# Kernel optimization log

Measured on AMD Instinct MI355X. Metric: run time of the kernel, lower is better.

## Reference

```python
import jax, jax.numpy as jnp
import numpy as np

N = 100000
E = 1600000
IN_F = 128
OUT_F = 64
ALPHA = 0.2  # leaky relu slope
EPS = 1e-16


def setup_inputs() -> dict:
    key = jax.random.key(0)
    k1, k2, k3, k4 = jax.random.split(key, 4)
    x = jax.random.normal(k1, (N, IN_F), dtype=jnp.float32)
    edge_index = jax.random.randint(k2, (2, E), 0, N, dtype=jnp.int64)
    # xavier_uniform with gain=1.414
    gain = 1.414
    limW = gain * np.sqrt(6.0 / (IN_F + OUT_F))
    W = jax.random.uniform(k3, (IN_F, OUT_F), minval=-limW, maxval=limW, dtype=jnp.float32)
    lima = gain * np.sqrt(6.0 / (2 * OUT_F + 1))
    a = jax.random.uniform(k4, (2 * OUT_F, 1), minval=-lima, maxval=lima, dtype=jnp.float32)
    return {"x": x, "edge_index": edge_index, "W": W, "a": a}


def reference(x, edge_index, W, a):
    src = edge_index[0]
    tgt = edge_index[1]
    Wh = x @ W  # (N, out)
    # e = leakyrelu([Wh[src] || Wh[tgt]] @ a) ; split a to avoid materializing concat
    a_src = a[:OUT_F, 0]
    a_tgt = a[OUT_F:, 0]
    score_src = Wh @ a_src  # (N,)
    score_tgt = Wh @ a_tgt  # (N,)
    e = jax.nn.leaky_relu(score_src[src] + score_tgt[tgt], ALPHA)  # (E,)
    # segment softmax over edges grouped by target node
    e_max = jax.ops.segment_max(e, tgt, num_segments=N)  # -inf for empty segments, never gathered
    e_exp = jnp.exp(e - e_max[tgt])
    e_sum = jax.ops.segment_sum(e_exp, tgt, num_segments=N)
    alpha = e_exp / (e_sum[tgt] + EPS)  # (E,)
    # dropout is identity in eval mode
    v_weighted = Wh[src] * alpha[:, None]  # (E, out)
    h_prime = jax.ops.segment_sum(v_weighted, tgt, num_segments=N)  # (N, out)
    return jax.nn.elu(h_prime)  # concat=True branch
```

## Files before the change

kernel.cpp:

```cpp
#include <hip/hip_runtime.h>

#define N_NODES 100000
#define N_EDGES 1600000
#define IN_FEAT 128
#define OUT_FEAT 64
#define LRELU_SLOPE 0.2f
#define EPS_DENOM 1e-16f

#define SB_SHIFT 8
#define SB_NODES 256
#define NSB 391
#define N_SUB 8
#define SUBA_CAP 704
#define STAGE_CAP 4608
#define CH 4096
#define SCAT_BLOCKS ((N_EDGES + CH - 1) / CH)
#define GEMM_BLOCKS ((N_NODES + 63) / 64)

typedef __attribute__((ext_vector_type(8))) short bf16x8;
typedef __attribute__((ext_vector_type(4))) float f32x4;

__device__ __forceinline__ unsigned int enc_f(float x) {
    unsigned int u = __float_as_uint(x);
    return (u & 0x80000000u) ? ~u : (u | 0x80000000u);
}
__device__ __forceinline__ float dec_f(unsigned int u) {
    u = (u & 0x80000000u) ? (u ^ 0x80000000u) : ~u;
    return __uint_as_float(u);
}
#define ENC_NEG_INF 0x007FFFFFu

__device__ __forceinline__ unsigned short f2bf(float f) {
    unsigned int u = __float_as_uint(f);
    u = (u + 0x7FFFu + ((u >> 16) & 1u)) >> 16;
    return (unsigned short)u;
}

__global__ __launch_bounds__(256) void init_prep_kernel(
    const float* __restrict__ W, int* __restrict__ cursorA,
    unsigned short* __restrict__ WTb)
{
    const int i = blockIdx.x * 256 + threadIdx.x;
    if (i < NSB * N_SUB) cursorA[i] = i * SUBA_CAP;
    if (i < OUT_FEAT * IN_FEAT) {
        const int n = i >> 7, k = i & 127;
        WTb[i] = f2bf(W[k * OUT_FEAT + n]);
    }
}

struct GemmS {
    unsigned short xs[64][136];
    float ssp[4][64];
    float stp[4][64];
};
struct ScatS {
    int staged[CH];
    int hcnt[NSB];
    int gbase[NSB];
    int lcnt[NSB];
    int lbase[NSB];
    int pfx[256];
};

__global__ __launch_bounds__(256) void gemm_scatter_kernel(
    const float* __restrict__ x, const unsigned short* __restrict__ WTb,
    const float* __restrict__ a, const int* __restrict__ ei,
    int* __restrict__ cursorA, int* __restrict__ bucketsA,
    unsigned short* __restrict__ WhB,
    float* __restrict__ s_src, float* __restrict__ s_tgt)
{
    __shared__ __align__(16) char smem[sizeof(ScatS) > sizeof(GemmS) ? sizeof(ScatS)
                                                                     : sizeof(GemmS)];
    const int tid = threadIdx.x;

    if (blockIdx.x < SCAT_BLOCKS) {
        ScatS& S = *(ScatS*)smem;
        const int base = blockIdx.x * CH;
        const int sub = blockIdx.x & (N_SUB - 1);
        for (int j = tid; j < NSB; j += 256) S.hcnt[j] = 0;
        __syncthreads();
        int tloc[CH / 256], sloc[CH / 256];
        #pragma unroll
        for (int k = 0; k < CH / 256; ++k) {
            const int i = base + k * 256 + tid;
            tloc[k] = (i < N_EDGES) ? ei[N_EDGES + i] : -1;
            sloc[k] = (i < N_EDGES) ? ei[i] : 0;
            if (tloc[k] >= 0) atomicAdd(&S.hcnt[tloc[k] >> SB_SHIFT], 1);
        }
        __syncthreads();
        int carry = 0;
        for (int c0 = 0; c0 < NSB; c0 += 256) {
            const int idx = c0 + tid;
            const int v = (idx < NSB) ? S.hcnt[idx] : 0;
            S.pfx[tid] = v;
            __syncthreads();
            for (int off = 1; off < 256; off <<= 1) {
                const int add = (tid >= off) ? S.pfx[tid - off] : 0;
                __syncthreads();
                S.pfx[tid] += add;
                __syncthreads();
            }
            if (idx < NSB) S.lbase[idx] = carry + S.pfx[tid] - v;
            carry += S.pfx[255];
            __syncthreads();
        }
        for (int j = tid; j < NSB; j += 256) {
            S.lcnt[j] = 0;
            const int c = S.hcnt[j];
            S.gbase[j] = c ? atomicAdd(&cursorA[j * N_SUB + sub], c) : 0;
        }
        __syncthreads();
        #pragma unroll
        for (int k = 0; k < CH / 256; ++k) {
            if (tloc[k] >= 0) {
                const int sb = tloc[k] >> SB_SHIFT;
                const int r = atomicAdd(&S.lcnt[sb], 1);
                S.staged[S.lbase[sb] + r] = sloc[k] | ((tloc[k] & (SB_NODES - 1)) << 17);
            }
        }
        __syncthreads();
        const int grp = tid >> 4, gl = tid & 15;
        for (int sb = grp; sb < NSB; sb += 16) {
            const int c = S.hcnt[sb];
            const int lb = S.lbase[sb];
            const int gb = S.gbase[sb];
            for (int k = gl; k < c; k += 16) bucketsA[gb + k] = S.staged[lb + k];
        }
        return;
    }

    GemmS& G = *(GemmS*)smem;
    const int wid = tid >> 6, lane = tid & 63;
    const int r0 = (blockIdx.x - SCAT_BLOCKS) * 64;

    #pragma unroll
    for (int it = 0; it < 8; ++it) {
        const int idx4 = it * 256 + tid;
        const int row = idx4 >> 5;
        const int col = (idx4 & 31) * 4;
        float4 v = make_float4(0.f, 0.f, 0.f, 0.f);
        if (r0 + row < N_NODES) v = *(const float4*)(x + (size_t)(r0 + row) * IN_FEAT + col);
        const unsigned int p0 = (unsigned int)f2bf(v.x) | ((unsigned int)f2bf(v.y) << 16);
        const unsigned int p1 = (unsigned int)f2bf(v.z) | ((unsigned int)f2bf(v.w) << 16);
        *(uint2*)&G.xs[row][col] = make_uint2(p0, p1);
    }
    __syncthreads();

    const int cgrp = lane >> 4;
    const int cl = lane & 15;
    const int col = wid * 16 + cl;
    f32x4 acc0 = {0.f,0.f,0.f,0.f}, acc1 = acc0, acc2 = acc0, acc3 = acc0;
    #pragma unroll
    for (int kb = 0; kb < IN_FEAT; kb += 32) {
        const bf16x8 bfrag = *(const bf16x8*)(WTb + col * IN_FEAT + kb + cgrp * 8);
        const bf16x8 a0 = *(const bf16x8*)&G.xs[ 0 + cl][kb + cgrp * 8];
        const bf16x8 a1 = *(const bf16x8*)&G.xs[16 + cl][kb + cgrp * 8];
        const bf16x8 a2 = *(const bf16x8*)&G.xs[32 + cl][kb + cgrp * 8];
        const bf16x8 a3 = *(const bf16x8*)&G.xs[48 + cl][kb + cgrp * 8];
        acc0 = __builtin_amdgcn_mfma_f32_16x16x32_bf16(a0, bfrag, acc0, 0, 0, 0);
        acc1 = __builtin_amdgcn_mfma_f32_16x16x32_bf16(a1, bfrag, acc1, 0, 0, 0);
        acc2 = __builtin_amdgcn_mfma_f32_16x16x32_bf16(a2, bfrag, acc2, 0, 0, 0);
        acc3 = __builtin_amdgcn_mfma_f32_16x16x32_bf16(a3, bfrag, acc3, 0, 0, 0);
    }

    const float a_s = a[col], a_t = a[OUT_FEAT + col];
    #pragma unroll
    for (int mt = 0; mt < 4; ++mt) {
        const f32x4 av = (mt == 0) ? acc0 : (mt == 1) ? acc1 : (mt == 2) ? acc2 : acc3;
        #pragma unroll
        for (int r = 0; r < 4; ++r) {
            const int lrow = mt * 16 + cgrp * 4 + r;
            const float v = av[r];
            const int grow = r0 + lrow;
            if (grow < N_NODES) WhB[(size_t)grow * OUT_FEAT + col] = f2bf(v);
            float ss = v * a_s;
            float st = v * a_t;
            #pragma unroll
            for (int off = 1; off < 16; off <<= 1) {
                ss += __shfl_xor(ss, off, 64);
                st += __shfl_xor(st, off, 64);
            }
            if (cl == 0) { G.ssp[wid][lrow] = ss; G.stp[wid][lrow] = st; }
        }
    }
    __syncthreads();
    if (tid < 64 && r0 + tid < N_NODES) {
        s_src[r0 + tid] = (G.ssp[0][tid] + G.ssp[1][tid]) + (G.ssp[2][tid] + G.ssp[3][tid]);
        s_tgt[r0 + tid] = (G.stp[0][tid] + G.stp[1][tid]) + (G.stp[2][tid] + G.stp[3][tid]);
    }
}

__global__ __launch_bounds__(512) void sort_aggr_kernel(
    const int* __restrict__ cursorA, const int* __restrict__ bucketsA,
    const float* __restrict__ s_src, const float* __restrict__ s_tgt,
    const unsigned short* __restrict__ WhB, float* __restrict__ out)
{
    __shared__ int2 stage[STAGE_CAP];
    __shared__ int2 sorted[STAGE_CAP];
    __shared__ float stgt[SB_NODES];
    __shared__ int cnt[SB_NODES];
    __shared__ int pfx[SB_NODES];
    __shared__ int cur[SB_NODES];
    __shared__ unsigned int m_enc[SB_NODES];
    __shared__ int c_ofs[N_SUB + 1];
    const int b = blockIdx.x;
    const int tid = threadIdx.x;

    if (tid < SB_NODES) {
        cnt[tid] = 0;
        m_enc[tid] = ENC_NEG_INF;
        const int node = b * SB_NODES + tid;
        stgt[tid] = (node < N_NODES) ? s_tgt[node] : 0.0f;
    }
    if (tid == 0) {
        int o = 0;
        #pragma unroll
        for (int s = 0; s < N_SUB; ++s) {
            c_ofs[s] = o;
            o += cursorA[b * N_SUB + s] - (b * N_SUB + s) * SUBA_CAP;
        }
        c_ofs[N_SUB] = o;
    }
    __syncthreads();
    const int tot = c_ofs[N_SUB];
    #pragma unroll
    for (int s = 0; s < N_SUB; ++s) {
        const int o = c_ofs[s];
        const int c = c_ofs[s + 1] - o;
        const int* src = bucketsA + (size_t)(b * N_SUB + s) * SUBA_CAP;
        for (int k = tid; k < c; k += 512) {
            const int pk = src[k];
            const int tl = (pk >> 17) & (SB_NODES - 1);
            float v = s_src[pk & 0x1FFFF] + stgt[tl];
            v = (v >= 0.0f) ? v : LRELU_SLOPE * v;
            stage[o + k] = make_int2(pk, __float_as_int(v));
            atomicAdd(&cnt[tl], 1);
            atomicMax(&m_enc[tl], enc_f(v));
        }
    }
    __syncthreads();
    if (tid < SB_NODES) pfx[tid] = cnt[tid];
    __syncthreads();
    for (int off = 1; off < SB_NODES; off <<= 1) {
        const int add = (tid < SB_NODES && tid >= off) ? pfx[tid - off] : 0;
        __syncthreads();
        if (tid < SB_NODES) pfx[tid] += add;
        __syncthreads();
    }
    if (tid < SB_NODES) {
        const int ex = pfx[tid] - cnt[tid];
        cur[tid] = ex;
        pfx[tid] = ex;
    }
    __syncthreads();
    for (int i = tid; i < tot; i += 512) {
        const int2 pk = stage[i];
        const int tl = (pk.x >> 17) & (SB_NODES - 1);
        const int pos = atomicAdd(&cur[tl], 1);
        const float w = __expf(__int_as_float(pk.y) - dec_f(m_enc[tl]));
        sorted[pos] = make_int2(pk.x & 0x1FFFF, __float_as_int(w));
    }
    __syncthreads();

    const int grp = tid >> 4, gl = tid & 15;
    const char* whb = (const char*)WhB;
    const unsigned int foff = (unsigned int)gl << 3;
    #pragma unroll
    for (int n = 0; n < 8; ++n) {
        const int nl = grp * 8 + n;
        const int node = b * SB_NODES + nl;
        if (node >= N_NODES) continue;
        const int beg = pfx[nl];
        const int end = beg + cnt[nl];
        float a0 = 0.f, a1 = 0.f, a2 = 0.f, a3 = 0.f, sum = 0.f;
        int i = beg;
        for (; i + 4 <= end; i += 4) {
            const int2 p0 = sorted[i],     p1 = sorted[i + 1];
            const int2 p2 = sorted[i + 2], p3 = sorted[i + 3];
            const uint2 g0 = *(const uint2*)(whb + (((unsigned int)p0.x << 7) + foff));
            const uint2 g1 = *(const uint2*)(whb + (((unsigned int)p1.x << 7) + foff));
            const uint2 g2 = *(const uint2*)(whb + (((unsigned int)p2.x << 7) + foff));
            const uint2 g3 = *(const uint2*)(whb + (((unsigned int)p3.x << 7) + foff));
            const float w0 = __int_as_float(p0.y), w1 = __int_as_float(p1.y);
            const float w2 = __int_as_float(p2.y), w3 = __int_as_float(p3.y);
            a0 += w0 * __uint_as_float(g0.x << 16) + w1 * __uint_as_float(g1.x << 16)
                + w2 * __uint_as_float(g2.x << 16) + w3 * __uint_as_float(g3.x << 16);
            a1 += w0 * __uint_as_float(g0.x & 0xFFFF0000u) + w1 * __uint_as_float(g1.x & 0xFFFF0000u)
                + w2 * __uint_as_float(g2.x & 0xFFFF0000u) + w3 * __uint_as_float(g3.x & 0xFFFF0000u);
            a2 += w0 * __uint_as_float(g0.y << 16) + w1 * __uint_as_float(g1.y << 16)
                + w2 * __uint_as_float(g2.y << 16) + w3 * __uint_as_float(g3.y << 16);
            a3 += w0 * __uint_as_float(g0.y & 0xFFFF0000u) + w1 * __uint_as_float(g1.y & 0xFFFF0000u)
                + w2 * __uint_as_float(g2.y & 0xFFFF0000u) + w3 * __uint_as_float(g3.y & 0xFFFF0000u);
            sum += (w0 + w1) + (w2 + w3);
        }
        for (; i < end; ++i) {
            const int2 pk = sorted[i];
            const uint2 g0 = *(const uint2*)(whb + (((unsigned int)pk.x << 7) + foff));
            const float w0 = __int_as_float(pk.y);
            a0 += w0 * __uint_as_float(g0.x << 16);
            a1 += w0 * __uint_as_float(g0.x & 0xFFFF0000u);
            a2 += w0 * __uint_as_float(g0.y << 16);
            a3 += w0 * __uint_as_float(g0.y & 0xFFFF0000u);
            sum += w0;
        }
        const float inv = 1.0f / (sum + EPS_DENOM);
        float4 o;
        o.x = a0 * inv; o.y = a1 * inv; o.z = a2 * inv; o.w = a3 * inv;
        o.x = (o.x > 0.f) ? o.x : expm1f(o.x);
        o.y = (o.y > 0.f) ? o.y : expm1f(o.y);
        o.z = (o.z > 0.f) ? o.z : expm1f(o.z);
        o.w = (o.w > 0.f) ? o.w : expm1f(o.w);
        *(float4*)(out + (size_t)node * OUT_FEAT + (gl << 2)) = o;
    }
}

extern "C" void kernel_launch(void* const* d_in, const int* in_sizes, int n_in,
                              void* d_out, int out_size, void* d_ws, size_t ws_size,
                              hipStream_t stream) {
    const float* x  = (const float*)d_in[0];
    const int*   ei = (const int*)d_in[1];
    const float* W  = (const float*)d_in[2];
    const float* a  = (const float*)d_in[3];
    float* out = (float*)d_out;

    char* p = (char*)d_ws;
    unsigned short* WhB = (unsigned short*)p; p += (size_t)N_NODES * OUT_FEAT * 2;
    unsigned short* WTb = (unsigned short*)p; p += (size_t)OUT_FEAT * IN_FEAT * 2;
    float* s_src    = (float*)p;  p += (size_t)N_NODES * 4;
    float* s_tgt    = (float*)p;  p += (size_t)N_NODES * 4;
    int*   cursorA  = (int*)p;    p += (size_t)NSB * N_SUB * 4;
    p = (char*)(((size_t)p + 15) & ~(size_t)15);
    int*   bucketsA = (int*)p;    p += (size_t)NSB * N_SUB * SUBA_CAP * 4;

    init_prep_kernel<<<32, 256, 0, stream>>>(W, cursorA, WTb);
    gemm_scatter_kernel<<<SCAT_BLOCKS + GEMM_BLOCKS, 256, 0, stream>>>(
        x, WTb, a, ei, cursorA, bucketsA, WhB, s_src, s_tgt);
    sort_aggr_kernel<<<NSB, 512, 0, stream>>>(cursorA, bucketsA, s_src, s_tgt, WhB, out);
}
```

Baseline: 96.55 us.

## Replace LDS scans with wave-shuffle scans and drop staging buffer via recompute

Both block-level prefix sums (the scatter kernel's histogram scan and the aggregation kernel's per-node count scan) now use wavefront shuffle scans plus a small cross-wave sum, instead of log-step LDS scans with two barriers per step. The aggregation kernel no longer keeps a 36 KB stage buffer. It re-reads the bucket entries and recomputes the leaky-relu scores in a second pass. This halves LDS use so more blocks can be resident per CU, and removes many barriers. The cost is a second global read of the buckets and the s_src gathers.

```diff
diff --git a/kernel.cpp b/kernel.cpp
--- a/kernel.cpp
+++ b/kernel.cpp
@@ -92,16 +92,18 @@
         for (int c0 = 0; c0 < NSB; c0 += 256) {
             const int idx = c0 + tid;
             const int v = (idx < NSB) ? S.hcnt[idx] : 0;
-            S.pfx[tid] = v;
+            int incl = v;
+            #pragma unroll
+            for (int off = 1; off < 64; off <<= 1) {
+                const int t = __shfl_up(incl, off, 64);
+                if ((tid & 63) >= off) incl += t;
+            }
+            if ((tid & 63) == 63) S.pfx[tid >> 6] = incl;
             __syncthreads();
-            for (int off = 1; off < 256; off <<= 1) {
-                const int add = (tid >= off) ? S.pfx[tid - off] : 0;
-                __syncthreads();
-                S.pfx[tid] += add;
-                __syncthreads();
-            }
-            if (idx < NSB) S.lbase[idx] = carry + S.pfx[tid] - v;
-            carry += S.pfx[255];
+            int wpre = 0;
+            for (int wv = 0; wv < (tid >> 6); ++wv) wpre += S.pfx[wv];
+            if (idx < NSB) S.lbase[idx] = carry + wpre + incl - v;
+            carry += S.pfx[0] + S.pfx[1] + S.pfx[2] + S.pfx[3];
             __syncthreads();
         }
         for (int j = tid; j < NSB; j += 256) {
@@ -195,14 +197,14 @@
     const float* __restrict__ s_src, const float* __restrict__ s_tgt,
     const unsigned short* __restrict__ WhB, float* __restrict__ out)
 {
-    __shared__ int2 stage[STAGE_CAP];
     __shared__ int2 sorted[STAGE_CAP];
     __shared__ float stgt[SB_NODES];
     __shared__ int cnt[SB_NODES];
     __shared__ int pfx[SB_NODES];
     __shared__ int cur[SB_NODES];
     __shared__ unsigned int m_enc[SB_NODES];
-    __shared__ int c_ofs[N_SUB + 1];
+    __shared__ int scnt[N_SUB];
+    __shared__ int wsum[4];
     const int b = blockIdx.x;
     const int tid = threadIdx.x;
 
@@ -212,53 +214,58 @@
         const int node = b * SB_NODES + tid;
         stgt[tid] = (node < N_NODES) ? s_tgt[node] : 0.0f;
     }
-    if (tid == 0) {
-        int o = 0;
-        #pragma unroll
-        for (int s = 0; s < N_SUB; ++s) {
-            c_ofs[s] = o;
-            o += cursorA[b * N_SUB + s] - (b * N_SUB + s) * SUBA_CAP;
-        }
-        c_ofs[N_SUB] = o;
-    }
-    __syncthreads();
-    const int tot = c_ofs[N_SUB];
+    if (tid < N_SUB) scnt[tid] = cursorA[b * N_SUB + tid] - (b * N_SUB + tid) * SUBA_CAP;
+    __syncthreads();
+
     #pragma unroll
     for (int s = 0; s < N_SUB; ++s) {
-        const int o = c_ofs[s];
-        const int c = c_ofs[s + 1] - o;
+        const int c = scnt[s];
         const int* src = bucketsA + (size_t)(b * N_SUB + s) * SUBA_CAP;
         for (int k = tid; k < c; k += 512) {
             const int pk = src[k];
             const int tl = (pk >> 17) & (SB_NODES - 1);
             float v = s_src[pk & 0x1FFFF] + stgt[tl];
             v = (v >= 0.0f) ? v : LRELU_SLOPE * v;
-            stage[o + k] = make_int2(pk, __float_as_int(v));
             atomicAdd(&cnt[tl], 1);
             atomicMax(&m_enc[tl], enc_f(v));
         }
     }
     __syncthreads();
-    if (tid < SB_NODES) pfx[tid] = cnt[tid];
-    __syncthreads();
-    for (int off = 1; off < SB_NODES; off <<= 1) {
-        const int add = (tid < SB_NODES && tid >= off) ? pfx[tid - off] : 0;
-        __syncthreads();
-        if (tid < SB_NODES) pfx[tid] += add;
-        __syncthreads();
-    }
+
+    int vv = 0, incl = 0;
     if (tid < SB_NODES) {
-        const int ex = pfx[tid] - cnt[tid];
+        vv = cnt[tid];
+        incl = vv;
+        #pragma unroll
+        for (int off = 1; off < 64; off <<= 1) {
+            const int t = __shfl_up(incl, off, 64);
+            if ((tid & 63) >= off) incl += t;
+        }
+        if ((tid & 63) == 63) wsum[tid >> 6] = incl;
+    }
+    __syncthreads();
+    if (tid < SB_NODES) {
+        int wpre = 0;
+        for (int wv = 0; wv < (tid >> 6); ++wv) wpre += wsum[wv];
+        const int ex = wpre + incl - vv;
+        pfx[tid] = ex;
         cur[tid] = ex;
-        pfx[tid] = ex;
-    }
-    __syncthreads();
-    for (int i = tid; i < tot; i += 512) {
-        const int2 pk = stage[i];
-        const int tl = (pk.x >> 17) & (SB_NODES - 1);
-        const int pos = atomicAdd(&cur[tl], 1);
-        const float w = __expf(__int_as_float(pk.y) - dec_f(m_enc[tl]));
-        sorted[pos] = make_int2(pk.x & 0x1FFFF, __float_as_int(w));
+    }
+    __syncthreads();
+
+    #pragma unroll
+    for (int s = 0; s < N_SUB; ++s) {
+        const int c = scnt[s];
+        const int* src = bucketsA + (size_t)(b * N_SUB + s) * SUBA_CAP;
+        for (int k = tid; k < c; k += 512) {
+            const int pk = src[k];
+            const int tl = (pk >> 17) & (SB_NODES - 1);
+            float v = s_src[pk & 0x1FFFF] + stgt[tl];
+            v = (v >= 0.0f) ? v : LRELU_SLOPE * v;
+            const int pos = atomicAdd(&cur[tl], 1);
+            const float w = __expf(v - dec_f(m_enc[tl]));
+            sorted[pos] = make_int2(pk & 0x1FFFF, __float_as_int(w));
+        }
     }
     __syncthreads();
 
```

New measurement: 101.4 us. 5.0% more time.
